# Performance work log

Measured on AMD Instinct MI355X. Metric: run time of the kernel, lower is better.

Reference implementation:

```python
import jax, jax.numpy as jnp
import numpy as np
from jax import lax

B, T, HID = 2, 2048, 2048
H, DK, DV = 16, 64, 128          # num_heads, head_k_dim, head_v_dim
C = 16                            # chunk_size (hardcoded in module __call__)
LOWR = 16                         # gate_low_rank_dim
NORMALIZER = 16.0                 # gate_logit_normalizer
EPS = 1e-5
SCALE = DK ** -0.5


def setup_inputs() -> dict:
    key = jax.random.key(0)
    ks = jax.random.split(key, 9)
    def w(k, shape):
        return jax.random.normal(k, shape, jnp.float32) * (shape[0] ** -0.5)
    return {
        "hidden_states": jax.random.normal(ks[0], (B, T, HID), jnp.float32),
        "Wq": w(ks[1], (HID, H * DK)),
        "Wk": w(ks[2], (HID, H * DK)),
        "Wv": w(ks[3], (HID, H * DV)),
        "Wg": w(ks[4], (HID, H * DV)),
        "Wgk1": w(ks[5], (HID, LOWR)),
        "Wgk2": w(ks[6], (LOWR, H * DK)),
        "bgk2": jnp.zeros((H * DK,), jnp.float32),
        "Wo": w(ks[7], (H * DV, HID)),
        "norm_w": jnp.ones((DV,), jnp.float32),
    }


def _chunk_gla(q, k, v, gk):
    """Chunked gated linear attention.
    q,k,gk: [B,T,H,DK], v: [B,T,H,DV]; gk is log-decay (<= 0).
    Recurrence: S_t = diag(exp(gk_t)) S_{t-1} + k_t^T v_t ; o_t = scale * q_t S_t.
    """
    b, t, h, dk = q.shape
    dv = v.shape[-1]
    n = t // C
    def to_chunks(x):  # [B,T,H,d] -> [B,H,N,C,d]
        return x.reshape(b, n, C, h, x.shape[-1]).transpose(0, 3, 1, 2, 4)
    q, k, v, gk = map(to_chunks, (q, k, v, gk))

    gc = jnp.cumsum(gk, axis=3)                 # within-chunk cumulative log-decay
    qe = q * jnp.exp(gc) * SCALE                # decay-weighted queries
    ke = k * jnp.exp(-gc)                       # inverse-decay keys (safe for C=16)
    # intra-chunk causal attention: A[i,j] = sum_d q_i k_j exp(gc_i - gc_j), j<=i
    A = jnp.einsum('bhncd,bhnmd->bhncm', qe, ke)
    A = jnp.where(jnp.tril(jnp.ones((C, C), bool)), A, 0.0)
    o_intra = jnp.einsum('bhncm,bhnme->bhnce', A, v)

    g_last = gc[:, :, :, -1:, :]                # [B,H,N,1,DK]
    k_dec = k * jnp.exp(g_last - gc)            # keys decayed to end of chunk
    kv = jnp.einsum('bhncd,bhnce->bhnde', k_dec, v)   # per-chunk state increment
    decay = jnp.exp(g_last[:, :, :, 0, :])      # [B,H,N,DK] total chunk decay

    def step(S, inp):  # S: [B,H,DK,DV]
        qe_c, kv_c, dec_c = inp
        o_c = jnp.einsum('bhcd,bhde->bhce', qe_c, S)
        return dec_c[..., None] * S + kv_c, o_c

    S0 = jnp.zeros((b, h, dk, dv), q.dtype)
    xs = (qe.transpose(2, 0, 1, 3, 4), kv.transpose(2, 0, 1, 3, 4), decay.transpose(2, 0, 1, 3))
    _, o_inter = lax.scan(step, S0, xs)          # [N,B,H,C,DV]

    o = o_intra + o_inter.transpose(1, 2, 0, 3, 4)
    return o.transpose(0, 2, 3, 1, 4).reshape(b, t, h, dv)  # [B,T,H,DV]


def reference(hidden_states, Wq, Wk, Wv, Wg, Wgk1, Wgk2, bgk2, Wo, norm_w):
    x = hidden_states
    q = (x @ Wq).reshape(B, T, H, DK)
    k = (x @ Wk).reshape(B, T, H, DK)
    v = (x @ Wv).reshape(B, T, H, DV)
    gk = jax.nn.log_sigmoid((x @ Wgk1) @ Wgk2 + bgk2) / NORMALIZER
    gk = gk.reshape(B, T, H, DK)

    o = _chunk_gla(q, k, v, gk)                  # [B,T,H,DV]

    # FusedRMSNormGated: rmsnorm(o) * weight, gated by swish(g) per head
    g = (x @ Wg).reshape(B, T, H, DV)
    o = o * lax.rsqrt(jnp.mean(o * o, axis=-1, keepdims=True) + EPS) * norm_w
    o = o * (g * jax.nn.sigmoid(g))
    return o.reshape(B, T, H * DV) @ Wo
```

## Files before the change

### kernel.cpp

```cpp
#include <hip/hip_runtime.h>
#include <hip/hip_bf16.h>
#include <math.h>

#define B_    2
#define T_    2048
#define HID_  2048
#define H_    16
#define DK_   64
#define DV_   128
#define CC    16
#define NCHUNK (T_/CC)
#define NSEG  16
#define M_    (B_*T_)
#define SCALE_ 0.125f

typedef __attribute__((ext_vector_type(8))) __bf16 bf16x8;
typedef __attribute__((ext_vector_type(8))) unsigned short u16x8;
typedef __attribute__((ext_vector_type(4))) float f32x4;

__device__ __forceinline__ unsigned short f2bf(float f) {
  unsigned int u = __float_as_uint(f);
  u += 0x7fff + ((u >> 16) & 1);
  return (unsigned short)(u >> 16);
}
__device__ __forceinline__ float bf2f(unsigned short u) {
  return __uint_as_float(((unsigned int)u) << 16);
}

typedef const __attribute__((address_space(1))) void* as1cv;
typedef __attribute__((address_space(3))) void* as3v;
__device__ __forceinline__ void gload16(const void* g, void* l) {
  __builtin_amdgcn_global_load_lds((as1cv)g, (as3v)l, 16, 0, 0);
}

__global__ __launch_bounds__(256) void prep_kernel(const float* __restrict__ x,
                                                   unsigned short* __restrict__ xb,
                                                   const float* __restrict__ Wq,
                                                   const float* __restrict__ Wk,
                                                   const float* __restrict__ Wv,
                                                   const float* __restrict__ Wg,
                                                   const float* __restrict__ Wo,
                                                   unsigned short* __restrict__ WqkT,
                                                   unsigned short* __restrict__ WvgT,
                                                   unsigned short* __restrict__ WoT) {
  const int t = threadIdx.x;
  int id = blockIdx.x;
  if (id < 2048) {
    const float4* x4 = reinterpret_cast<const float4*>(x);
    ushort4* o4 = reinterpret_cast<ushort4*>(xb);
    const int base = id * 1024 + t;
    float4 f0 = x4[base];
    float4 f1 = x4[base + 256];
    float4 f2 = x4[base + 512];
    float4 f3 = x4[base + 768];
    ushort4 u0 = {f2bf(f0.x), f2bf(f0.y), f2bf(f0.z), f2bf(f0.w)};
    ushort4 u1 = {f2bf(f1.x), f2bf(f1.y), f2bf(f1.z), f2bf(f1.w)};
    ushort4 u2 = {f2bf(f2.x), f2bf(f2.y), f2bf(f2.z), f2bf(f2.w)};
    ushort4 u3 = {f2bf(f3.x), f2bf(f3.y), f2bf(f3.z), f2bf(f3.w)};
    o4[base] = u0; o4[base + 256] = u1; o4[base + 512] = u2; o4[base + 768] = u3;
    return;
  }
  id -= 2048;
  const float* in; unsigned short* out; int N;
  if (id < 512)        { in = Wq; out = WqkT;                         N = 1024; }
  else if (id < 1024)  { in = Wk; out = WqkT + (size_t)1024*2048;     N = 1024; id -= 512; }
  else if (id < 2048)  { in = Wv; out = WvgT;                         N = 2048; id -= 1024; }
  else if (id < 3072)  { in = Wg; out = WvgT + (size_t)2048*2048;     N = 2048; id -= 2048; }
  else                 { in = Wo; out = WoT;                          N = 2048; id -= 3072; }
  const int nx = N / 64;
  const int n0 = (id % nx) * 64;
  const int k0 = (id / nx) * 64;
  __shared__ float tl[64][65];
  const int kr = t >> 4;
  const int nq = t & 15;
  #pragma unroll
  for (int it = 0; it < 4; ++it) {
    int kk = it*16 + kr;
    float4 v = *reinterpret_cast<const float4*>(&in[(size_t)(k0 + kk) * N + n0 + nq*4]);
    tl[kk][nq*4+0] = v.x; tl[kk][nq*4+1] = v.y;
    tl[kk][nq*4+2] = v.z; tl[kk][nq*4+3] = v.w;
  }
  __syncthreads();
  const int nr = t >> 3;
  const int kq = t & 7;
  #pragma unroll
  for (int it = 0; it < 2; ++it) {
    int nn = it*32 + nr;
    u16x8 u;
    #pragma unroll
    for (int r = 0; r < 8; ++r) u[r] = f2bf(tl[kq*8 + r][nn]);
    *reinterpret_cast<u16x8*>(&out[(size_t)(n0 + nn) * 2048 + k0 + kq*8]) = u;
  }
}

__global__ __launch_bounds__(256) void lr_kernel(const float* __restrict__ x,
                                                 const float* __restrict__ w1,
                                                 const float* __restrict__ w2,
                                                 const float* __restrict__ bias,
                                                 float* __restrict__ gkout) {
  const int row0 = blockIdx.x * 4;
  const int t = threadIdx.x;
  __shared__ float part[4][4][17];
  __shared__ float t1s[4][16];
  const int r    = t >> 6;
  const int lane = t & 63;
  const int j    = lane & 15;
  const int p    = lane >> 4;
  const float* xr = x + (size_t)(row0 + r) * HID_;
  float acc = 0.f;
  const int k0 = p * 512;
  for (int kk = k0; kk < k0 + 512; kk += 4) {
    float4 xv = *reinterpret_cast<const float4*>(&xr[kk]);
    acc = fmaf(xv.x, w1[(kk+0)*16 + j], acc);
    acc = fmaf(xv.y, w1[(kk+1)*16 + j], acc);
    acc = fmaf(xv.z, w1[(kk+2)*16 + j], acc);
    acc = fmaf(xv.w, w1[(kk+3)*16 + j], acc);
  }
  part[r][p][j] = acc;
  __syncthreads();
  if (t < 64) {
    int rr = t >> 4, jj = t & 15;
    t1s[rr][jj] = part[rr][0][jj] + part[rr][1][jj] + part[rr][2][jj] + part[rr][3][jj];
  }
  __syncthreads();
  #pragma unroll
  for (int i = 0; i < 4; ++i) {
    int n = t + i * 256;
    float b0 = bias[n];
    float a0 = b0, a1 = b0, a2 = b0, a3 = b0;
    #pragma unroll
    for (int jj = 0; jj < 16; ++jj) {
      float wv = w2[jj * 1024 + n];
      a0 = fmaf(t1s[0][jj], wv, a0);
      a1 = fmaf(t1s[1][jj], wv, a1);
      a2 = fmaf(t1s[2][jj], wv, a2);
      a3 = fmaf(t1s[3][jj], wv, a3);
    }
    gkout[(size_t)(row0+0)*1024 + n] = (fminf(a0,0.f) - log1pf(expf(-fabsf(a0)))) * (1.f/16.f);
    gkout[(size_t)(row0+1)*1024 + n] = (fminf(a1,0.f) - log1pf(expf(-fabsf(a1)))) * (1.f/16.f);
    gkout[(size_t)(row0+2)*1024 + n] = (fminf(a2,0.f) - log1pf(expf(-fabsf(a2)))) * (1.f/16.f);
    gkout[(size_t)(row0+3)*1024 + n] = (fminf(a3,0.f) - log1pf(expf(-fabsf(a3)))) * (1.f/16.f);
  }
}

template<bool OBF>
__global__ __launch_bounds__(512, 2) void gemm256(const unsigned short* __restrict__ A,
                                                  const unsigned short* __restrict__ Bt,
                                                  void* __restrict__ Cv,
                                                  int M, int N, int K) {
  __shared__ char ldsb[131072];
  const int t    = threadIdx.x;
  const int lane = t & 63;
  const int wid  = t >> 6;
  const int wr   = wid >> 2;
  const int wc   = wid & 3;
  const int lr   = lane & 15;
  const int lk   = lane >> 4;
  int flat = blockIdx.y * gridDim.x + blockIdx.x;
  if (gridDim.x * gridDim.y == 256) flat = (flat & 7) * 32 + (flat >> 3);
  const int row0 = (flat / gridDim.x) * 256;
  const int col0 = (flat % gridDim.x) * 256;
  const int NKT  = K >> 6;
  const size_t K2 = (size_t)K * 2;

  const int r_s  = t >> 2;
  const int kx_s = ((t & 3) * 16) ^ (((t >> 5) & 1) << 5);

  const int ha = wr;
  const int hb = wc >> 1;
  const int rbl = (wc & 1) * 64;

  f32x4 acc[8][4];
  #pragma unroll
  for (int m = 0; m < 8; ++m)
    #pragma unroll
    for (int n = 0; n < 4; ++n) acc[m][n] = (f32x4){0.f, 0.f, 0.f, 0.f};

  auto stage_half = [&](int p, int o, int h, int kt) {
    const char* src = o ? (const char*)Bt : (const char*)A;
    const int R0 = (o ? col0 : row0) + h * 128;
    const char* g = src + (size_t)(R0 + r_s) * K2 + (size_t)kt * 128 + kx_s;
    char* l = ldsb + ((((p << 1) | o) << 1 | h) << 14) + t * 16;
    gload16(g, l);
    gload16(g + 64, l + 8192);
  };
  auto lda = [&](int p, int mf, int ks) -> bf16x8 {
    int r = mf * 16 + lr;
    int a = ((((p << 1) | 0) << 1 | ha) << 14) + ks * 8192 + r * 64 + lk * 16;
    a ^= ((r >> 3) & 1) << 5;
    return *(const bf16x8*)(ldsb + a);
  };
  auto ldb = [&](int p, int nf, int ks) -> bf16x8 {
    int r = rbl + nf * 16 + lr;
    int a = ((((p << 1) | 1) << 1 | hb) << 14) + ks * 8192 + r * 64 + lk * 16;
    a ^= ((r >> 3) & 1) << 5;
    return *(const bf16x8*)(ldsb + a);
  };

  stage_half(0, 1, 0, 0); stage_half(0, 1, 1, 0);
  stage_half(0, 0, 0, 0); stage_half(0, 0, 1, 0);
  if (1 < NKT) {
    stage_half(1, 1, 0, 1); stage_half(1, 1, 1, 1);
    stage_half(1, 0, 0, 1); stage_half(1, 0, 1, 1);
  }
  asm volatile("s_waitcnt vmcnt(8)" ::: "memory");
  __builtin_amdgcn_s_barrier();
  __builtin_amdgcn_sched_barrier(0);

  bf16x8 fa[4][2], fb[2][2], fb2[2][2];

  for (int kt = 0; kt < NKT; ++kt) {
    const int p = kt & 1;
    const bool st = (kt + 2 < NKT);
    #pragma unroll
    for (int m = 0; m < 4; ++m) { fa[m][0] = lda(p, m, 0); fa[m][1] = lda(p, m, 1); }
    #pragma unroll
    for (int n = 0; n < 2; ++n) { fb[n][0] = ldb(p, n, 0); fb[n][1] = ldb(p, n, 1); }
    #pragma unroll
    for (int n = 0; n < 2; ++n) { fb2[n][0] = ldb(p, n + 2, 0); fb2[n][1] = ldb(p, n + 2, 1); }
    __builtin_amdgcn_s_setprio(1);
    #pragma unroll
    for (int m = 0; m < 4; ++m)
      #pragma unroll
      for (int n = 0; n < 2; ++n) {
        acc[m][n] = __builtin_amdgcn_mfma_f32_16x16x32_bf16(fa[m][0], fb[n][0], acc[m][n], 0, 0, 0);
        acc[m][n] = __builtin_amdgcn_mfma_f32_16x16x32_bf16(fa[m][1], fb[n][1], acc[m][n], 0, 0, 0);
      }
    #pragma unroll
    for (int m = 0; m < 4; ++m)
      #pragma unroll
      for (int n = 0; n < 2; ++n) {
        acc[m][n+2] = __builtin_amdgcn_mfma_f32_16x16x32_bf16(fa[m][0], fb2[n][0], acc[m][n+2], 0, 0, 0);
        acc[m][n+2] = __builtin_amdgcn_mfma_f32_16x16x32_bf16(fa[m][1], fb2[n][1], acc[m][n+2], 0, 0, 0);
      }
    __builtin_amdgcn_s_setprio(0);
    __builtin_amdgcn_sched_barrier(0);
    __builtin_amdgcn_s_barrier();
    __builtin_amdgcn_sched_barrier(0);
    if (st) { stage_half(p, 1, 0, kt + 2); stage_half(p, 1, 1, kt + 2); }
    #pragma unroll
    for (int m = 0; m < 4; ++m) { fa[m][0] = lda(p, m + 4, 0); fa[m][1] = lda(p, m + 4, 1); }
    __builtin_amdgcn_s_setprio(1);
    #pragma unroll
    for (int m = 0; m < 4; ++m)
      #pragma unroll
      for (int n = 0; n < 2; ++n) {
        acc[m+4][n] = __builtin_amdgcn_mfma_f32_16x16x32_bf16(fa[m][0], fb[n][0], acc[m+4][n], 0, 0, 0);
        acc[m+4][n] = __builtin_amdgcn_mfma_f32_16x16x32_bf16(fa[m][1], fb[n][1], acc[m+4][n], 0, 0, 0);
      }
    #pragma unroll
    for (int m = 0; m < 4; ++m)
      #pragma unroll
      for (int n = 0; n < 2; ++n) {
        acc[m+4][n+2] = __builtin_amdgcn_mfma_f32_16x16x32_bf16(fa[m][0], fb2[n][0], acc[m+4][n+2], 0, 0, 0);
        acc[m+4][n+2] = __builtin_amdgcn_mfma_f32_16x16x32_bf16(fa[m][1], fb2[n][1], acc[m+4][n+2], 0, 0, 0);
      }
    __builtin_amdgcn_s_setprio(0);
    __builtin_amdgcn_sched_barrier(0);
    __builtin_amdgcn_s_barrier();
    __builtin_amdgcn_sched_barrier(0);
    if (st) { stage_half(p, 0, 0, kt + 2); stage_half(p, 0, 1, kt + 2); }
    if (kt == NKT - 2) asm volatile("s_waitcnt vmcnt(0)" ::: "memory");
    else               asm volatile("s_waitcnt vmcnt(8)" ::: "memory");
    __builtin_amdgcn_s_barrier();
    __builtin_amdgcn_sched_barrier(0);
  }

  #pragma unroll
  for (int m = 0; m < 8; ++m) {
    int row = row0 + wr*128 + m*16 + lk*4;
    #pragma unroll
    for (int n = 0; n < 4; ++n) {
      int col = col0 + wc*64 + n*16 + lr;
      #pragma unroll
      for (int j = 0; j < 4; ++j) {
        if (OBF) ((unsigned short*)Cv)[(size_t)(row + j) * N + col] = f2bf(acc[m][n][j]);
        else     ((float*)Cv)[(size_t)(row + j) * N + col] = acc[m][n][j];
      }
    }
  }
}

template<bool OBF>
__global__ __launch_bounds__(512, 2) void gemm256x128(const unsigned short* __restrict__ A,
                                                      const unsigned short* __restrict__ Bt,
                                                      void* __restrict__ Cv,
                                                      int M, int N, int K) {
  __shared__ char ldsb[98304];
  const int t    = threadIdx.x;
  const int lane = t & 63;
  const int wid  = t >> 6;
  const int wr   = wid >> 1;
  const int wc   = wid & 1;
  const int lr   = lane & 15;
  const int lk   = lane >> 4;
  int flat = blockIdx.y * gridDim.x + blockIdx.x;
  if (gridDim.x * gridDim.y == 256) flat = (flat & 7) * 32 + (flat >> 3);
  const int row0 = (flat / gridDim.x) * 256;
  const int col0 = (flat % gridDim.x) * 128;
  const int NKT  = K >> 6;
  const size_t K2 = (size_t)K * 2;

  const int r_s  = t >> 2;
  const int kx_s = ((t & 3) * 16) ^ (((t >> 5) & 1) << 5);

  const int ha  = wr >> 1;
  const int ral = (wr & 1) * 64;
  const int rbl = wc * 64;

  f32x4 acc[4][4];
  #pragma unroll
  for (int m = 0; m < 4; ++m)
    #pragma unroll
    for (int n = 0; n < 4; ++n) acc[m][n] = (f32x4){0.f, 0.f, 0.f, 0.f};

  auto stage_slot = [&](int p, int slot, int kt) {
    const char* src = (slot == 2) ? (const char*)Bt : (const char*)A;
    const int R0 = (slot == 2) ? col0 : (row0 + slot * 128);
    const char* g = src + (size_t)(R0 + r_s) * K2 + (size_t)kt * 128 + kx_s;
    char* l = ldsb + p * 49152 + slot * 16384 + t * 16;
    gload16(g, l);
    gload16(g + 64, l + 8192);
  };
  auto lda = [&](int p, int mf, int ks) -> bf16x8 {
    int r = ral + mf * 16 + lr;
    int a = p * 49152 + ha * 16384 + ks * 8192 + r * 64 + lk * 16;
    a ^= ((r >> 3) & 1) << 5;
    return *(const bf16x8*)(ldsb + a);
  };
  auto ldb = [&](int p, int nf, int ks) -> bf16x8 {
    int r = rbl + nf * 16 + lr;
    int a = p * 49152 + 32768 + ks * 8192 + r * 64 + lk * 16;
    a ^= ((r >> 3) & 1) << 5;
    return *(const bf16x8*)(ldsb + a);
  };

  stage_slot(0, 2, 0); stage_slot(0, 0, 0); stage_slot(0, 1, 0);
  if (1 < NKT) { stage_slot(1, 2, 1); stage_slot(1, 0, 1); stage_slot(1, 1, 1); }
  asm volatile("s_waitcnt vmcnt(6)" ::: "memory");
  __builtin_amdgcn_s_barrier();
  __builtin_amdgcn_sched_barrier(0);

  bf16x8 fa[2][2], fb[2][2], fb2[2][2];

  for (int kt = 0; kt < NKT; ++kt) {
    const int p = kt & 1;
    const bool st = (kt + 2 < NKT);
    #pragma unroll
    for (int m = 0; m < 2; ++m) { fa[m][0] = lda(p, m, 0); fa[m][1] = lda(p, m, 1); }
    #pragma unroll
    for (int n = 0; n < 2; ++n) { fb[n][0] = ldb(p, n, 0); fb[n][1] = ldb(p, n, 1); }
    #pragma unroll
    for (int n = 0; n < 2; ++n) { fb2[n][0] = ldb(p, n + 2, 0); fb2[n][1] = ldb(p, n + 2, 1); }
    __builtin_amdgcn_s_setprio(1);
    #pragma unroll
    for (int m = 0; m < 2; ++m)
      #pragma unroll
      for (int n = 0; n < 2; ++n) {
        acc[m][n] = __builtin_amdgcn_mfma_f32_16x16x32_bf16(fa[m][0], fb[n][0], acc[m][n], 0, 0, 0);
        acc[m][n] = __builtin_amdgcn_mfma_f32_16x16x32_bf16(fa[m][1], fb[n][1], acc[m][n], 0, 0, 0);
      }
    #pragma unroll
    for (int m = 0; m < 2; ++m)
      #pragma unroll
      for (int n = 0; n < 2; ++n) {
        acc[m][n+2] = __builtin_amdgcn_mfma_f32_16x16x32_bf16(fa[m][0], fb2[n][0], acc[m][n+2], 0, 0, 0);
        acc[m][n+2] = __builtin_amdgcn_mfma_f32_16x16x32_bf16(fa[m][1], fb2[n][1], acc[m][n+2], 0, 0, 0);
      }
    __builtin_amdgcn_s_setprio(0);
    __builtin_amdgcn_sched_barrier(0);
    __builtin_amdgcn_s_barrier();
    __builtin_amdgcn_sched_barrier(0);
    if (st) stage_slot(p, 2, kt + 2);
    #pragma unroll
    for (int m = 0; m < 2; ++m) { fa[m][0] = lda(p, m + 2, 0); fa[m][1] = lda(p, m + 2, 1); }
    __builtin_amdgcn_s_setprio(1);
    #pragma unroll
    for (int m = 0; m < 2; ++m)
      #pragma unroll
      for (int n = 0; n < 2; ++n) {
        acc[m+2][n] = __builtin_amdgcn_mfma_f32_16x16x32_bf16(fa[m][0], fb[n][0], acc[m+2][n], 0, 0, 0);
        acc[m+2][n] = __builtin_amdgcn_mfma_f32_16x16x32_bf16(fa[m][1], fb[n][1], acc[m+2][n], 0, 0, 0);
      }
    #pragma unroll
    for (int m = 0; m < 2; ++m)
      #pragma unroll
      for (int n = 0; n < 2; ++n) {
        acc[m+2][n+2] = __builtin_amdgcn_mfma_f32_16x16x32_bf16(fa[m][0], fb2[n][0], acc[m+2][n+2], 0, 0, 0);
        acc[m+2][n+2] = __builtin_amdgcn_mfma_f32_16x16x32_bf16(fa[m][1], fb2[n][1], acc[m+2][n+2], 0, 0, 0);
      }
    __builtin_amdgcn_s_setprio(0);
    __builtin_amdgcn_sched_barrier(0);
    __builtin_amdgcn_s_barrier();
    __builtin_amdgcn_sched_barrier(0);
    if (st) { stage_slot(p, 0, kt + 2); stage_slot(p, 1, kt + 2); }
    if (kt == NKT - 2) asm volatile("s_waitcnt vmcnt(0)" ::: "memory");
    else               asm volatile("s_waitcnt vmcnt(6)" ::: "memory");
    __builtin_amdgcn_s_barrier();
    __builtin_amdgcn_sched_barrier(0);
  }

  #pragma unroll
  for (int m = 0; m < 4; ++m) {
    int row = row0 + wr*64 + m*16 + lk*4;
    #pragma unroll
    for (int n = 0; n < 4; ++n) {
      int col = col0 + wc*64 + n*16 + lr;
      #pragma unroll
      for (int j = 0; j < 4; ++j) {
        if (OBF) ((unsigned short*)Cv)[(size_t)(row + j) * N + col] = f2bf(acc[m][n][j]);
        else     ((float*)Cv)[(size_t)(row + j) * N + col] = acc[m][n][j];
      }
    }
  }
}

__global__ __launch_bounds__(256) void gla_phase_a(const unsigned short* __restrict__ qkb,
                                                   const unsigned short* __restrict__ vg,
                                                   const float* __restrict__ gk,
                                                   float* __restrict__ Sseg,
                                                   float* __restrict__ Dseg) {
  const int seg = blockIdx.x & 15;
  const int h   = (blockIdx.x >> 4) & 15;
  const int b   = blockIdx.x >> 8;
  const int t    = threadIdx.x;
  const int lane = t & 63;
  const int wid  = t >> 6;
  const int q    = lane >> 4;
  const int lr   = lane & 15;
  __shared__ float gc[16][68];
  __shared__ float dec_[64];
  __shared__ unsigned short kdT[64][40];
  __shared__ unsigned short vvT[128][40];

  for (int i = t; i < 1024; i += 256) kdT[i >> 4][16 + (i & 15)] = 0;
  for (int i = t; i < 2048; i += 256) vvT[i >> 4][16 + (i & 15)] = 0;

  f32x4 s_reg[2][4];
  #pragma unroll
  for (int et = 0; et < 2; ++et)
    #pragma unroll
    for (int dt = 0; dt < 4; ++dt) s_reg[et][dt] = (f32x4){0.f,0.f,0.f,0.f};
  float gt = 0.f;

  for (int c8 = 0; c8 < NCHUNK/NSEG; ++c8) {
    const int ch = seg * (NCHUNK/NSEG) + c8;
    __syncthreads();
    {
      float acc = 0.f;
      #pragma unroll
      for (int c = 0; c < CC; ++c) {
        acc += gk[((size_t)(b*T_ + ch*CC + c)) * 1024 + h*DK_ + lane];
        gc[c][lane] = acc;
      }
      gt += acc;
      dec_[lane] = expf(acc);
    }
    __syncthreads();
    {
      int c = t >> 4, d0 = (t & 15) * 4;
      ushort4 k4u = *reinterpret_cast<const ushort4*>(
          &qkb[((size_t)(b*T_ + ch*CC + c)) * 2048 + 1024 + h*DK_ + d0]);
      float ka[4] = {bf2f(k4u.x), bf2f(k4u.y), bf2f(k4u.z), bf2f(k4u.w)};
      #pragma unroll
      for (int j = 0; j < 4; ++j)
        kdT[d0 + j][c] = f2bf(ka[j] * expf(gc[CC-1][d0 + j] - gc[c][d0 + j]));
    }
    {
      int c = t & 15, e0 = (t >> 4) * 8;
      const ushort4* vp = reinterpret_cast<const ushort4*>(
          &vg[((size_t)(b*T_ + ch*CC + c)) * 4096 + h*DV_ + e0]);
      ushort4 a = vp[0], bb = vp[1];
      vvT[e0+0][c] = a.x;  vvT[e0+1][c] = a.y;  vvT[e0+2][c] = a.z;  vvT[e0+3][c] = a.w;
      vvT[e0+4][c] = bb.x; vvT[e0+5][c] = bb.y; vvT[e0+6][c] = bb.z; vvT[e0+7][c] = bb.w;
    }
    __syncthreads();
    bf16x8 vf[2], kf[4];
    #pragma unroll
    for (int et = 0; et < 2; ++et)
      vf[et] = *(const bf16x8*)&vvT[wid*32 + et*16 + lr][q*8];
    #pragma unroll
    for (int dt = 0; dt < 4; ++dt)
      kf[dt] = *(const bf16x8*)&kdT[dt*16 + lr][q*8];
    #pragma unroll
    for (int et = 0; et < 2; ++et)
      #pragma unroll
      for (int dt = 0; dt < 4; ++dt) {
        f32x4 dl = __builtin_amdgcn_mfma_f32_16x16x32_bf16(vf[et], kf[dt],
                     (f32x4){0.f,0.f,0.f,0.f}, 0, 0, 0);
        float dv = dec_[dt*16 + lr];
        #pragma unroll
        for (int j = 0; j < 4; ++j)
          s_reg[et][dt][j] = fmaf(s_reg[et][dt][j], dv, dl[j]);
      }
  }
  const size_t base = ((size_t)((b*H_ + h)*NSEG + seg)) * (DK_*DV_);
  #pragma unroll
  for (int et = 0; et < 2; ++et)
    #pragma unroll
    for (int dt = 0; dt < 4; ++dt)
      #pragma unroll
      for (int j = 0; j < 4; ++j)
        Sseg[base + (size_t)(wid*32 + et*16 + q*4 + j) * 64 + dt*16 + lr] = s_reg[et][dt][j];
  if (t < 64)
    Dseg[(size_t)((b*H_ + h)*NSEG + seg) * DK_ + t] = expf(gt);
}

__global__ __launch_bounds__(256) void gla_combine(float* __restrict__ Sseg,
                                                   const float* __restrict__ Dseg) {
  const int bh = blockIdx.x;
  const int t = threadIdx.x;
  __shared__ float Dl[64];
  float4 S_run[8];
  #pragma unroll
  for (int j = 0; j < 8; ++j) S_run[j] = (float4){0.f,0.f,0.f,0.f};
  const int d0 = (t * 4) & 63;
  for (int seg = 0; seg < NSEG; ++seg) {
    const size_t base = ((size_t)bh*NSEG + seg) * (DK_*DV_);
    if (t < 64) Dl[t] = Dseg[((size_t)bh*NSEG + seg) * DK_ + t];
    __syncthreads();
    #pragma unroll
    for (int j = 0; j < 8; ++j) {
      int idx = j*1024 + t*4;
      float4 sl = *reinterpret_cast<float4*>(&Sseg[base + idx]);
      *reinterpret_cast<float4*>(&Sseg[base + idx]) = S_run[j];
      S_run[j].x = fmaf(Dl[d0+0], S_run[j].x, sl.x);
      S_run[j].y = fmaf(Dl[d0+1], S_run[j].y, sl.y);
      S_run[j].z = fmaf(Dl[d0+2], S_run[j].z, sl.z);
      S_run[j].w = fmaf(Dl[d0+3], S_run[j].w, sl.w);
    }
    __syncthreads();
  }
}

__global__ __launch_bounds__(256) void gla_phase_c(const unsigned short* __restrict__ qkb,
                                                   const unsigned short* __restrict__ vg,
                                                   const float* __restrict__ gk,
                                                   const float* __restrict__ Sseg,
                                                   const float* __restrict__ norm_w,
                                                   unsigned short* __restrict__ yb) {
  const int seg = blockIdx.x & 15;
  const int h   = (blockIdx.x >> 4) & 15;
  const int b   = blockIdx.x >> 8;
  const int t    = threadIdx.x;
  const int lane = t & 63;
  const int wid  = t >> 6;
  const int q    = lane >> 4;
  const int lr   = lane & 15;
  __shared__ float gc[16][68];
  __shared__ float dec_[64];
  __shared__ unsigned short qe[16][72];
  __shared__ unsigned short ke[16][72];
  __shared__ unsigned short kdT[64][40];
  __shared__ unsigned short vvT[128][40];
  __shared__ unsigned short Am[16][40];
  __shared__ unsigned short Sb[128][72];
  __shared__ float ss_lds[4][16];
  __shared__ float nw[128];

  for (int i = t; i < 1024; i += 256) kdT[i >> 4][16 + (i & 15)] = 0;
  for (int i = t; i < 2048; i += 256) vvT[i >> 4][16 + (i & 15)] = 0;
  if (t < 256) { int c = t >> 4, m = t & 15; Am[c][16 + m] = 0; }
  if (t < 128) nw[t] = norm_w[t];

  f32x4 s_reg[2][4];
  const size_t sbase = ((size_t)((b*H_ + h)*NSEG + seg)) * (DK_*DV_);
  #pragma unroll
  for (int et = 0; et < 2; ++et)
    #pragma unroll
    for (int dt = 0; dt < 4; ++dt)
      #pragma unroll
      for (int j = 0; j < 4; ++j) {
        int e = wid*32 + et*16 + q*4 + j, d = dt*16 + lr;
        float v = Sseg[sbase + (size_t)e * 64 + d];
        s_reg[et][dt][j] = v;
        Sb[e][d] = f2bf(v);
      }

  for (int c8 = 0; c8 < NCHUNK/NSEG; ++c8) {
    const int ch = seg * (NCHUNK/NSEG) + c8;
    __syncthreads();
    {
      float acc = 0.f;
      #pragma unroll
      for (int c = 0; c < CC; ++c) {
        acc += gk[((size_t)(b*T_ + ch*CC + c)) * 1024 + h*DK_ + lane];
        gc[c][lane] = acc;
      }
      dec_[lane] = expf(acc);
    }
    __syncthreads();
    {
      int c = t >> 4, d0 = (t & 15) * 4;
      const size_t gbq = ((size_t)(b*T_ + ch*CC + c)) * 2048 + h*DK_ + d0;
      ushort4 q4u = *reinterpret_cast<const ushort4*>(&qkb[gbq]);
      ushort4 k4u = *reinterpret_cast<const ushort4*>(&qkb[gbq + 1024]);
      float qa[4] = {bf2f(q4u.x), bf2f(q4u.y), bf2f(q4u.z), bf2f(q4u.w)};
      float ka[4] = {bf2f(k4u.x), bf2f(k4u.y), bf2f(k4u.z), bf2f(k4u.w)};
      ushort4 qw, kw;
      unsigned short* qwp = (unsigned short*)&qw;
      unsigned short* kwp = (unsigned short*)&kw;
      #pragma unroll
      for (int j = 0; j < 4; ++j) {
        float gcv = gc[c][d0 + j];
        float gl  = gc[CC-1][d0 + j];
        qwp[j] = f2bf(qa[j] * expf(gcv) * SCALE_);
        kwp[j] = f2bf(ka[j] * expf(-gcv));
        kdT[d0 + j][c] = f2bf(ka[j] * expf(gl - gcv));
      }
      *reinterpret_cast<ushort4*>(&qe[c][d0]) = qw;
      *reinterpret_cast<ushort4*>(&ke[c][d0]) = kw;
    }
    {
      int c = t & 15, e0 = (t >> 4) * 8;
      const ushort4* vp = reinterpret_cast<const ushort4*>(
          &vg[((size_t)(b*T_ + ch*CC + c)) * 4096 + h*DV_ + e0]);
      ushort4 a = vp[0], bb = vp[1];
      vvT[e0+0][c] = a.x;  vvT[e0+1][c] = a.y;  vvT[e0+2][c] = a.z;  vvT[e0+3][c] = a.w;
      vvT[e0+4][c] = bb.x; vvT[e0+5][c] = bb.y; vvT[e0+6][c] = bb.z; vvT[e0+7][c] = bb.w;
    }
    __syncthreads();
    bf16x8 qA0 = *(const bf16x8*)&qe[lr][q*8];
    bf16x8 qA1 = *(const bf16x8*)&qe[lr][32 + q*8];
    {
      bf16x8 kB0 = *(const bf16x8*)&ke[lr][q*8];
      bf16x8 kB1 = *(const bf16x8*)&ke[lr][32 + q*8];
      f32x4 accA = __builtin_amdgcn_mfma_f32_16x16x32_bf16(qA0, kB0,
                     (f32x4){0.f,0.f,0.f,0.f}, 0, 0, 0);
      accA = __builtin_amdgcn_mfma_f32_16x16x32_bf16(qA1, kB1, accA, 0, 0, 0);
      #pragma unroll
      for (int j = 0; j < 4; ++j) {
        int c = q*4 + j;
        Am[c][lr] = (lr <= c) ? f2bf(accA[j]) : (unsigned short)0;
      }
    }
    bf16x8 vf[2], kf[4];
    #pragma unroll
    for (int et = 0; et < 2; ++et)
      vf[et] = *(const bf16x8*)&vvT[wid*32 + et*16 + lr][q*8];
    #pragma unroll
    for (int dt = 0; dt < 4; ++dt)
      kf[dt] = *(const bf16x8*)&kdT[dt*16 + lr][q*8];
    #pragma unroll
    for (int et = 0; et < 2; ++et)
      #pragma unroll
      for (int dt = 0; dt < 4; ++dt) {
        f32x4 dl = __builtin_amdgcn_mfma_f32_16x16x32_bf16(vf[et], kf[dt],
                     (f32x4){0.f,0.f,0.f,0.f}, 0, 0, 0);
        float dv = dec_[dt*16 + lr];
        #pragma unroll
        for (int j = 0; j < 4; ++j)
          s_reg[et][dt][j] = fmaf(s_reg[et][dt][j], dv, dl[j]);
      }
    __syncthreads();
    {
      bf16x8 amA = *(const bf16x8*)&Am[lr][q*8];
      f32x4 accO[2];
      #pragma unroll
      for (int et = 0; et < 2; ++et) {
        int e0 = wid*32 + et*16;
        bf16x8 sB0 = *(const bf16x8*)&Sb[e0 + lr][q*8];
        bf16x8 sB1 = *(const bf16x8*)&Sb[e0 + lr][32 + q*8];
        accO[et] = __builtin_amdgcn_mfma_f32_16x16x32_bf16(qA0, sB0,
                     (f32x4){0.f,0.f,0.f,0.f}, 0, 0, 0);
        accO[et] = __builtin_amdgcn_mfma_f32_16x16x32_bf16(qA1, sB1, accO[et], 0, 0, 0);
        accO[et] = __builtin_amdgcn_mfma_f32_16x16x32_bf16(amA, vf[et], accO[et], 0, 0, 0);
      }
      #pragma unroll
      for (int j = 0; j < 4; ++j) {
        float pj = accO[0][j]*accO[0][j] + accO[1][j]*accO[1][j];
        pj += __shfl_xor(pj, 1, 64);
        pj += __shfl_xor(pj, 2, 64);
        pj += __shfl_xor(pj, 4, 64);
        pj += __shfl_xor(pj, 8, 64);
        if (lr == 0) ss_lds[wid][q*4 + j] = pj;
      }
      __syncthreads();
      #pragma unroll
      for (int j = 0; j < 4; ++j) {
        int r = q*4 + j;
        float tot = ss_lds[0][r] + ss_lds[1][r] + ss_lds[2][r] + ss_lds[3][r];
        float inv = rsqrtf(tot * (1.f/128.f) + 1e-5f);
        const size_t rowg = (size_t)(b*T_ + ch*CC + r);
        #pragma unroll
        for (int et = 0; et < 2; ++et) {
          int e = wid*32 + et*16 + lr;
          float gv = bf2f(vg[rowg * 4096 + 2048 + h*DV_ + e]);
          float si = gv / (1.f + expf(-gv));
          yb[rowg * 2048 + h*DV_ + e] = f2bf(accO[et][j] * inv * nw[e] * si);
        }
      }
    }
    __syncthreads();
    #pragma unroll
    for (int et = 0; et < 2; ++et)
      #pragma unroll
      for (int dt = 0; dt < 4; ++dt)
        #pragma unroll
        for (int j = 0; j < 4; ++j)
          Sb[wid*32 + et*16 + q*4 + j][dt*16 + lr] = f2bf(s_reg[et][dt][j]);
  }
}

extern "C" void kernel_launch(void* const* d_in, const int* in_sizes, int n_in,
                              void* d_out, int out_size, void* d_ws, size_t ws_size,
                              hipStream_t stream) {
  const float* x      = (const float*)d_in[0];
  const float* Wq     = (const float*)d_in[1];
  const float* Wk     = (const float*)d_in[2];
  const float* Wv     = (const float*)d_in[3];
  const float* Wg     = (const float*)d_in[4];
  const float* Wgk1   = (const float*)d_in[5];
  const float* Wgk2   = (const float*)d_in[6];
  const float* bgk2   = (const float*)d_in[7];
  const float* Wo     = (const float*)d_in[8];
  const float* norm_w = (const float*)d_in[9];
  float* out = (float*)d_out;
  float* ws  = (float*)d_ws;

  unsigned short* qkb  = (unsigned short*)ws;
  float*          gkb  = ws + 8388608;
  unsigned short* vg   = (unsigned short*)(ws + 12582912);
  float*          wbuf = ws + 20971520;
  float*          Sseg = ws + 29360128;
  float*          Dseg = ws + 33554432;
  unsigned short* WoT  = (unsigned short*)(ws + 33652736);

  unsigned short* WqkT = (unsigned short*)wbuf;
  unsigned short* WvgT = (unsigned short*)(wbuf + 2097152);
  unsigned short* xb   = (unsigned short*)(wbuf + 6291456);
  unsigned short* yb   = (unsigned short*)wbuf;

  dim3 blk(256);
  prep_kernel<<<dim3(6144), blk, 0, stream>>>(x, xb, Wq, Wk, Wv, Wg, Wo, WqkT, WvgT, WoT);
  lr_kernel<<<dim3(1024), blk, 0, stream>>>(x, Wgk1, Wgk2, bgk2, gkb);
  gemm256x128<true ><<<dim3(2048/128, 4096/256), dim3(512), 0, stream>>>(xb, WqkT, qkb, M_, 2048, HID_);
  gemm256<true     ><<<dim3(4096/256, 4096/256), dim3(512), 0, stream>>>(xb, WvgT, vg, M_, 4096, HID_);
  gla_phase_a<<<B_*H_*NSEG, blk, 0, stream>>>(qkb, vg, gkb, Sseg, Dseg);
  gla_combine<<<B_*H_, blk, 0, stream>>>(Sseg, Dseg);
  gla_phase_c<<<B_*H_*NSEG, blk, 0, stream>>>(qkb, vg, gkb, Sseg, norm_w, yb);
  gemm256x128<false><<<dim3(2048/128, 4096/256), dim3(512), 0, stream>>>(yb, WoT, out, M_, HID_, HID_);
}
```

Before: 291.2 us.

## Interleave LDS fragment loads with MFMA phases and merge staging barriers in GEMMs

Restructures the inner K-loop of both GEMM kernels. LDS fragment reads are split by k-substep and issued ahead of the MFMA groups, with explicit lgkmcnt waits so compute overlaps outstanding shared-memory reads. Both halves of the next-tile global staging are now issued after a single mid-iteration barrier, which removes one workgroup barrier per iteration. The hand-tuned wait counts are fragile, and issuing all staging at once changes how pressure on memory and LDS is spread across the iteration.

```diff
diff --git a/kernel.cpp b/kernel.cpp
--- a/kernel.cpp
+++ b/kernel.cpp
@@ -207,61 +207,72 @@
   __builtin_amdgcn_s_barrier();
   __builtin_amdgcn_sched_barrier(0);
 
-  bf16x8 fa[4][2], fb[2][2], fb2[2][2];
+  bf16x8 fa[4][2], fb[4][2];
 
   for (int kt = 0; kt < NKT; ++kt) {
     const int p = kt & 1;
     const bool st = (kt + 2 < NKT);
     #pragma unroll
-    for (int m = 0; m < 4; ++m) { fa[m][0] = lda(p, m, 0); fa[m][1] = lda(p, m, 1); }
-    #pragma unroll
-    for (int n = 0; n < 2; ++n) { fb[n][0] = ldb(p, n, 0); fb[n][1] = ldb(p, n, 1); }
-    #pragma unroll
-    for (int n = 0; n < 2; ++n) { fb2[n][0] = ldb(p, n + 2, 0); fb2[n][1] = ldb(p, n + 2, 1); }
+    for (int m = 0; m < 4; ++m) fa[m][0] = lda(p, m, 0);
+    #pragma unroll
+    for (int n = 0; n < 4; ++n) fb[n][0] = ldb(p, n, 0);
+    #pragma unroll
+    for (int m = 0; m < 4; ++m) fa[m][1] = lda(p, m, 1);
+    #pragma unroll
+    for (int n = 0; n < 4; ++n) fb[n][1] = ldb(p, n, 1);
+    asm volatile("s_waitcnt lgkmcnt(8)" ::: "memory");
+    __builtin_amdgcn_sched_barrier(0);
     __builtin_amdgcn_s_setprio(1);
     #pragma unroll
     for (int m = 0; m < 4; ++m)
       #pragma unroll
-      for (int n = 0; n < 2; ++n) {
+      for (int n = 0; n < 4; ++n)
         acc[m][n] = __builtin_amdgcn_mfma_f32_16x16x32_bf16(fa[m][0], fb[n][0], acc[m][n], 0, 0, 0);
+    __builtin_amdgcn_s_setprio(0);
+    __builtin_amdgcn_sched_barrier(0);
+    #pragma unroll
+    for (int m = 0; m < 4; ++m) fa[m][0] = lda(p, m + 4, 0);
+    asm volatile("s_waitcnt lgkmcnt(4)" ::: "memory");
+    __builtin_amdgcn_sched_barrier(0);
+    __builtin_amdgcn_s_setprio(1);
+    #pragma unroll
+    for (int m = 0; m < 4; ++m)
+      #pragma unroll
+      for (int n = 0; n < 4; ++n)
         acc[m][n] = __builtin_amdgcn_mfma_f32_16x16x32_bf16(fa[m][1], fb[n][1], acc[m][n], 0, 0, 0);
-      }
+    __builtin_amdgcn_s_setprio(0);
+    __builtin_amdgcn_sched_barrier(0);
+    #pragma unroll
+    for (int m = 0; m < 4; ++m) fa[m][1] = lda(p, m + 4, 1);
+    asm volatile("s_waitcnt lgkmcnt(4)" ::: "memory");
+    __builtin_amdgcn_sched_barrier(0);
+    __builtin_amdgcn_s_setprio(1);
     #pragma unroll
     for (int m = 0; m < 4; ++m)
       #pragma unroll
-      for (int n = 0; n < 2; ++n) {
-        acc[m][n+2] = __builtin_amdgcn_mfma_f32_16x16x32_bf16(fa[m][0], fb2[n][0], acc[m][n+2], 0, 0, 0);
-        acc[m][n+2] = __builtin_amdgcn_mfma_f32_16x16x32_bf16(fa[m][1], fb2[n][1], acc[m][n+2], 0, 0, 0);
-      }
+      for (int n = 0; n < 4; ++n)
+        acc[m+4][n] = __builtin_amdgcn_mfma_f32_16x16x32_bf16(fa[m][0], fb[n][0], acc[m+4][n], 0, 0, 0);
     __builtin_amdgcn_s_setprio(0);
     __builtin_amdgcn_sched_barrier(0);
+    asm volatile("s_waitcnt lgkmcnt(0)" ::: "memory");
+    __builtin_amdgcn_sched_barrier(0);
     __builtin_amdgcn_s_barrier();
     __builtin_amdgcn_sched_barrier(0);
-    if (st) { stage_half(p, 1, 0, kt + 2); stage_half(p, 1, 1, kt + 2); }
-    #pragma unroll
-    for (int m = 0; m < 4; ++m) { fa[m][0] = lda(p, m + 4, 0); fa[m][1] = lda(p, m + 4, 1); }
+    if (st) {
+      stage_half(p, 1, 0, kt + 2); stage_half(p, 1, 1, kt + 2);
+      stage_half(p, 0, 0, kt + 2); stage_half(p, 0, 1, kt + 2);
+    }
     __builtin_amdgcn_s_setprio(1);
     #pragma unroll
     for (int m = 0; m < 4; ++m)
       #pragma unroll
-      for (int n = 0; n < 2; ++n) {
-        acc[m+4][n] = __builtin_amdgcn_mfma_f32_16x16x32_bf16(fa[m][0], fb[n][0], acc[m+4][n], 0, 0, 0);
+      for (int n = 0; n < 4; ++n)
         acc[m+4][n] = __builtin_amdgcn_mfma_f32_16x16x32_bf16(fa[m][1], fb[n][1], acc[m+4][n], 0, 0, 0);
-      }
-    #pragma unroll
-    for (int m = 0; m < 4; ++m)
-      #pragma unroll
-      for (int n = 0; n < 2; ++n) {
-        acc[m+4][n+2] = __builtin_amdgcn_mfma_f32_16x16x32_bf16(fa[m][0], fb2[n][0], acc[m+4][n+2], 0, 0, 0);
-        acc[m+4][n+2] = __builtin_amdgcn_mfma_f32_16x16x32_bf16(fa[m][1], fb2[n][1], acc[m+4][n+2], 0, 0, 0);
-      }
     __builtin_amdgcn_s_setprio(0);
     __builtin_amdgcn_sched_barrier(0);
-    __builtin_amdgcn_s_barrier();
-    __builtin_amdgcn_sched_barrier(0);
-    if (st) { stage_half(p, 0, 0, kt + 2); stage_half(p, 0, 1, kt + 2); }
     if (kt == NKT - 2) asm volatile("s_waitcnt vmcnt(0)" ::: "memory");
     else               asm volatile("s_waitcnt vmcnt(8)" ::: "memory");
+    __builtin_amdgcn_sched_barrier(0);
     __builtin_amdgcn_s_barrier();
     __builtin_amdgcn_sched_barrier(0);
   }
@@ -341,61 +352,69 @@
   __builtin_amdgcn_s_barrier();
   __builtin_amdgcn_sched_barrier(0);
 
-  bf16x8 fa[2][2], fb[2][2], fb2[2][2];
+  bf16x8 fa[2][2], fb[4][2];
 
   for (int kt = 0; kt < NKT; ++kt) {
     const int p = kt & 1;
     const bool st = (kt + 2 < NKT);
     #pragma unroll
-    for (int m = 0; m < 2; ++m) { fa[m][0] = lda(p, m, 0); fa[m][1] = lda(p, m, 1); }
-    #pragma unroll
-    for (int n = 0; n < 2; ++n) { fb[n][0] = ldb(p, n, 0); fb[n][1] = ldb(p, n, 1); }
-    #pragma unroll
-    for (int n = 0; n < 2; ++n) { fb2[n][0] = ldb(p, n + 2, 0); fb2[n][1] = ldb(p, n + 2, 1); }
+    for (int m = 0; m < 2; ++m) fa[m][0] = lda(p, m, 0);
+    #pragma unroll
+    for (int n = 0; n < 4; ++n) fb[n][0] = ldb(p, n, 0);
+    #pragma unroll
+    for (int m = 0; m < 2; ++m) fa[m][1] = lda(p, m, 1);
+    #pragma unroll
+    for (int n = 0; n < 4; ++n) fb[n][1] = ldb(p, n, 1);
+    asm volatile("s_waitcnt lgkmcnt(6)" ::: "memory");
+    __builtin_amdgcn_sched_barrier(0);
     __builtin_amdgcn_s_setprio(1);
     #pragma unroll
     for (int m = 0; m < 2; ++m)
       #pragma unroll
-      for (int n = 0; n < 2; ++n) {
+      for (int n = 0; n < 4; ++n)
         acc[m][n] = __builtin_amdgcn_mfma_f32_16x16x32_bf16(fa[m][0], fb[n][0], acc[m][n], 0, 0, 0);
+    __builtin_amdgcn_s_setprio(0);
+    __builtin_amdgcn_sched_barrier(0);
+    #pragma unroll
+    for (int m = 0; m < 2; ++m) fa[m][0] = lda(p, m + 2, 0);
+    asm volatile("s_waitcnt lgkmcnt(2)" ::: "memory");
+    __builtin_amdgcn_sched_barrier(0);
+    __builtin_amdgcn_s_setprio(1);
+    #pragma unroll
+    for (int m = 0; m < 2; ++m)
+      #pragma unroll
+      for (int n = 0; n < 4; ++n)
         acc[m][n] = __builtin_amdgcn_mfma_f32_16x16x32_bf16(fa[m][1], fb[n][1], acc[m][n], 0, 0, 0);
-      }
+    __builtin_amdgcn_s_setprio(0);
+    __builtin_amdgcn_sched_barrier(0);
+    #pragma unroll
+    for (int m = 0; m < 2; ++m) fa[m][1] = lda(p, m + 2, 1);
+    asm volatile("s_waitcnt lgkmcnt(2)" ::: "memory");
+    __builtin_amdgcn_sched_barrier(0);
+    __builtin_amdgcn_s_setprio(1);
     #pragma unroll
     for (int m = 0; m < 2; ++m)
       #pragma unroll
-      for (int n = 0; n < 2; ++n) {
-        acc[m][n+2] = __builtin_amdgcn_mfma_f32_16x16x32_bf16(fa[m][0], fb2[n][0], acc[m][n+2], 0, 0, 0);
-        acc[m][n+2] = __builtin_amdgcn_mfma_f32_16x16x32_bf16(fa[m][1], fb2[n][1], acc[m][n+2], 0, 0, 0);
-      }
+      for (int n = 0; n < 4; ++n)
+        acc[m+2][n] = __builtin_amdgcn_mfma_f32_16x16x32_bf16(fa[m][0], fb[n][0], acc[m+2][n], 0, 0, 0);
     __builtin_amdgcn_s_setprio(0);
     __builtin_amdgcn_sched_barrier(0);
+    asm volatile("s_waitcnt lgkmcnt(0)" ::: "memory");
+    __builtin_amdgcn_sched_barrier(0);
     __builtin_amdgcn_s_barrier();
     __builtin_amdgcn_sched_barrier(0);
-    if (st) stage_slot(p, 2, kt + 2);
-    #pragma unroll
-    for (int m = 0; m < 2; ++m) { fa[m][0] = lda(p, m + 2, 0); fa[m][1] = lda(p, m + 2, 1); }
+    if (st) { stage_slot(p, 2, kt + 2); stage_slot(p, 0, kt + 2); stage_slot(p, 1, kt + 2); }
     __builtin_amdgcn_s_setprio(1);
     #pragma unroll
     for (int m = 0; m < 2; ++m)
       #pragma unroll
-      for (int n = 0; n < 2; ++n) {
-        acc[m+2][n] = __builtin_amdgcn_mfma_f32_16x16x32_bf16(fa[m][0], fb[n][0], acc[m+2][n], 0, 0, 0);
+      for (int n = 0; n < 4; ++n)
         acc[m+2][n] = __builtin_amdgcn_mfma_f32_16x16x32_bf16(fa[m][1], fb[n][1], acc[m+2][n], 0, 0, 0);
-      }
-    #pragma unroll
-    for (int m = 0; m < 2; ++m)
-      #pragma unroll
-      for (int n = 0; n < 2; ++n) {
-        acc[m+2][n+2] = __builtin_amdgcn_mfma_f32_16x16x32_bf16(fa[m][0], fb2[n][0], acc[m+2][n+2], 0, 0, 0);
-        acc[m+2][n+2] = __builtin_amdgcn_mfma_f32_16x16x32_bf16(fa[m][1], fb2[n][1], acc[m+2][n+2], 0, 0, 0);
-      }
     __builtin_amdgcn_s_setprio(0);
     __builtin_amdgcn_sched_barrier(0);
-    __builtin_amdgcn_s_barrier();
-    __builtin_amdgcn_sched_barrier(0);
-    if (st) { stage_slot(p, 0, kt + 2); stage_slot(p, 1, kt + 2); }
     if (kt == NKT - 2) asm volatile("s_waitcnt vmcnt(0)" ::: "memory");
     else               asm volatile("s_waitcnt vmcnt(6)" ::: "memory");
+    __builtin_amdgcn_sched_barrier(0);
     __builtin_amdgcn_s_barrier();
     __builtin_amdgcn_sched_barrier(0);
   }
```

After: 300.1 us. +3.0%, slower.
